# Optimization experiments

Hardware: AMD Instinct MI355X
Metric: run time of the kernel (lower is better)

Reference implementation:

```python
import jax, jax.numpy as jnp
import numpy as np

N = 100000   # nodes
E = 800000   # edges
D_IN = 128   # input feature dim
H = 128      # GCN hidden units
M = 256      # MLP hidden
L = 40       # num_labels


def setup_inputs() -> dict:
    key = jax.random.key(0)
    ks = jax.random.split(key, 16)
    inp = {
        "x": jax.random.normal(ks[0], (N, D_IN), dtype=jnp.float32),
        "edge_index": jax.random.randint(ks[1], (2, E), 0, N, dtype=jnp.int32),
        "edge_weight": jax.random.uniform(ks[2], (E,), dtype=jnp.float32),
    }
    def glorot(k, shape):
        lim = np.sqrt(6.0 / (shape[0] + shape[1])).astype(np.float32)
        return jax.random.uniform(k, shape, jnp.float32, -lim, lim)
    inp["W0"] = glorot(ks[3], (D_IN, H)); inp["b0"] = jnp.zeros((H,), jnp.float32)
    inp["W1"] = glorot(ks[4], (H, H));    inp["b1"] = jnp.zeros((H,), jnp.float32)
    inp["W2"] = glorot(ks[5], (H, H));    inp["b2"] = jnp.zeros((H,), jnp.float32)
    inp["Wm0"] = glorot(ks[6], (H, M));   inp["bm0"] = jnp.zeros((M,), jnp.float32)
    inp["Wm1"] = glorot(ks[7], (M, L));   inp["bm1"] = jnp.zeros((L,), jnp.float32)
    return inp


def _gcn_norm(edge_index, edge_weight):
    # renorm trick: add self-loops (weight 1.0), then sym-normalize
    loop = jnp.arange(N, dtype=edge_index.dtype)
    row = jnp.concatenate([edge_index[0], loop])
    col = jnp.concatenate([edge_index[1], loop])
    w = jnp.concatenate([edge_weight, jnp.ones((N,), edge_weight.dtype)])
    deg = jax.ops.segment_sum(w, row, num_segments=N)
    dinv = jnp.where(deg > 0, jax.lax.rsqrt(deg), 0.0)
    norm = dinv[row] * w * dinv[col]
    return row, col, norm


def _gcn_layer(h, row, col, norm, W, b):
    h = h @ W                                   # [N, H]
    msg = h[col] * norm[:, None]                # gather + scale, [E+N, H]
    agg = jax.ops.segment_sum(msg, row, num_segments=N)
    return jax.nn.relu(agg + b)


def reference(x, edge_index, edge_weight, W0, b0, W1, b1, W2, b2, Wm0, bm0, Wm1, bm1):
    row, col, norm = _gcn_norm(edge_index, edge_weight)
    h = _gcn_layer(x, row, col, norm, W0, b0)
    h = _gcn_layer(h, row, col, norm, W1, b1)
    h = _gcn_layer(h, row, col, norm, W2, b2)
    h = jax.nn.relu(h @ Wm0 + bm0)              # MLP hidden
    return h @ Wm1 + bm1                        # logits [N, L]
```

## Files before the change

### kernel.cpp

```cpp
#include <hip/hip_runtime.h>
#include <hip/hip_fp16.h>
#include <math.h>

#define CAP 32
typedef unsigned short ushort_t;
typedef __attribute__((ext_vector_type(8))) short bf16x8;
typedef __attribute__((ext_vector_type(4))) float f32x4;

__device__ inline float bf2f_lo(unsigned u) { return __uint_as_float(u << 16); }
__device__ inline float bf2f_hi(unsigned u) { return __uint_as_float(u & 0xffff0000u); }
__device__ inline unsigned bf16rne(float f) {
    unsigned u = __float_as_uint(f);
    return (u + 0x7fffu + ((u >> 16) & 1u)) >> 16;
}
__device__ inline float dec_w(unsigned p) {
    return __half2float(__ushort_as_half((ushort_t)(p & 0x7fffu)));
}
__device__ inline bf16x8 u4_to_bf(uint4 u) {
    union { uint4 u; bf16x8 b; } cv; cv.u = u; return cv.b;
}
__device__ inline void accum8(float acc[8], uint4 u, float nm) {
    acc[0] = fmaf(bf2f_lo(u.x), nm, acc[0]);
    acc[1] = fmaf(bf2f_hi(u.x), nm, acc[1]);
    acc[2] = fmaf(bf2f_lo(u.y), nm, acc[2]);
    acc[3] = fmaf(bf2f_hi(u.y), nm, acc[3]);
    acc[4] = fmaf(bf2f_lo(u.z), nm, acc[4]);
    acc[5] = fmaf(bf2f_hi(u.z), nm, acc[5]);
    acc[6] = fmaf(bf2f_lo(u.w), nm, acc[6]);
    acc[7] = fmaf(bf2f_hi(u.w), nm, acc[7]);
}

__global__ __launch_bounds__(256) void k_setup0(const float* __restrict__ W0,
    ushort_t* __restrict__ W0t)
{
    int idx = blockIdx.x * 256 + threadIdx.x;
    if (idx < 128 * 128) {
        int k = idx >> 7, c = idx & 127;
        W0t[c * 128 + k] = (ushort_t)bf16rne(W0[idx]);
    }
}

__global__ __launch_bounds__(256) void k_prep2(const unsigned* __restrict__ bucket,
    const int* __restrict__ cursor, float* __restrict__ dinv, int n)
{
    int gid = blockIdx.x * 256 + threadIdx.x;
    int node = gid >> 4;
    if (node >= n) return;
    int f = gid & 15;
    int c = cursor[node]; if (c > CAP) c = CAP;
    float d = 0.f;
    int j0 = 2 * f;
    uint2 p = *(const uint2*)(bucket + (size_t)node * CAP + j0);
    if (j0 < c)     d += dec_w(p.x);
    if (j0 + 1 < c) d += dec_w(p.y);
    #pragma unroll
    for (int m = 1; m < 16; m <<= 1) d += __shfl_xor(d, m, 16);
    if (f == 0) dinv[node] = 1.0f / sqrtf(1.0f + d);
}

__global__ __launch_bounds__(256, 4) void k_fill_gemm1(
    const int* __restrict__ erow, const int* __restrict__ ecol,
    const float* __restrict__ ew, int* __restrict__ cursor,
    unsigned* __restrict__ bucket, int e,
    const float* __restrict__ x, const ushort_t* __restrict__ Wt,
    ushort_t* __restrict__ Cb, int n, int nbg, int K,
    const float* __restrict__ W1, const float* __restrict__ W2,
    const float* __restrict__ Wm0, const float* __restrict__ Wm1,
    ushort_t* __restrict__ W1t, ushort_t* __restrict__ W2t,
    ushort_t* __restrict__ Wm0t, ushort_t* __restrict__ Wm1t,
    int nbe_blk, int ntb)
{
    __shared__ ushort_t Wsb[128 * 128];
    const int tid = threadIdx.x;
    const int bid = blockIdx.x;
    if (bid % K != 0) {
        int fb = bid - bid / K - 1;
        if (fb < nbe_blk) {
            int i = fb * 256 + tid;
            if (i < e) {
                int r = erow[i];
                int pos = atomicAdd(&cursor[r], 1);
                if (pos < CAP) {
                    unsigned hb = (unsigned)__half_as_ushort(__float2half(ew[i]));
                    bucket[(size_t)r * CAP + pos] = ((unsigned)ecol[i] << 15) | hb;
                }
            }
        } else {
            const int S0 = 128 * 128, S1 = 128 * 256, S2 = 256 * 40;
            int total2 = 2 * S0 + S1 + S2;
            int tb = fb - nbe_blk;
            for (int idx = tb * 256 + tid; idx < total2; idx += ntb * 256) {
                int i = idx;
                const float* W; ushort_t* Wt2; int KK, NN;
                if (i < S0)            { W = W1;  Wt2 = W1t;  KK = 128; NN = 128; }
                else if (i < 2 * S0)   { W = W2;  Wt2 = W2t;  KK = 128; NN = 128; i -= S0; }
                else if (i < 2 * S0 + S1) { W = Wm0; Wt2 = Wm0t; KK = 128; NN = 256; i -= 2 * S0; }
                else                   { W = Wm1; Wt2 = Wm1t; KK = 256; NN = 40;  i -= 2 * S0 + S1; }
                int k = i / NN, c = i - k * NN;
                Wt2[(size_t)c * KK + k] = (ushort_t)bf16rne(W[(size_t)k * NN + c]);
            }
        }
        return;
    }
    const int gb = bid / K;
    if (gb >= nbg) return;
    const int row0 = gb * 128;
    {
        const int rl = tid >> 4, ch = tid & 15;
        #pragma unroll
        for (int it = 0; it < 8; ++it) {
            int c = it * 16 + rl;
            uint4 u = *(const uint4*)(Wt + (size_t)c * 128 + ch * 8);
            *(uint4*)&Wsb[(c * 128 + ch * 8) ^ ((c & 7) << 3)] = u;
        }
    }
    __syncthreads();

    const int lane = tid & 63;
    const int wv = tid >> 6;
    const int lm = lane & 15;
    const int lk = (lane >> 4) * 8;
    int g0 = row0 + wv * 32 + lm;
    int g1 = g0 + 16;
    size_t x0 = (size_t)((g0 < n) ? g0 : 0) * 128;
    size_t x1 = (size_t)((g1 < n) ? g1 : 0) * 128;

    f32x4 acc[2][8];
    #pragma unroll
    for (int m = 0; m < 2; ++m)
        #pragma unroll
        for (int t = 0; t < 8; ++t) acc[m][t] = (f32x4){0.f, 0.f, 0.f, 0.f};

    #pragma unroll
    for (int kk = 0; kk < 4; ++kk) {
        int k0 = kk * 32 + lk;
        const float4* s0 = (const float4*)(x + x0 + k0);
        const float4* s1 = (const float4*)(x + x1 + k0);
        float4 v0 = s0[0], v1 = s0[1], v2 = s1[0], v3 = s1[1];
        uint4 p0, p1;
        p0.x = bf16rne(v0.x) | (bf16rne(v0.y) << 16);
        p0.y = bf16rne(v0.z) | (bf16rne(v0.w) << 16);
        p0.z = bf16rne(v1.x) | (bf16rne(v1.y) << 16);
        p0.w = bf16rne(v1.z) | (bf16rne(v1.w) << 16);
        p1.x = bf16rne(v2.x) | (bf16rne(v2.y) << 16);
        p1.y = bf16rne(v2.z) | (bf16rne(v2.w) << 16);
        p1.z = bf16rne(v3.x) | (bf16rne(v3.y) << 16);
        p1.w = bf16rne(v3.z) | (bf16rne(v3.w) << 16);
        bf16x8 a0 = u4_to_bf(p0), a1 = u4_to_bf(p1);
        #pragma unroll
        for (int t = 0; t < 8; ++t) {
            int c = t * 16 + lm;
            bf16x8 b = *(const bf16x8*)&Wsb[(c * 128 + k0) ^ ((c & 7) << 3)];
            acc[0][t] = __builtin_amdgcn_mfma_f32_16x16x32_bf16(a0, b, acc[0][t], 0, 0, 0);
            acc[1][t] = __builtin_amdgcn_mfma_f32_16x16x32_bf16(a1, b, acc[1][t], 0, 0, 0);
        }
    }
    #pragma unroll
    for (int m = 0; m < 2; ++m) {
        #pragma unroll
        for (int j = 0; j < 4; ++j) {
            int gr = row0 + wv * 32 + m * 16 + (lane >> 4) * 4 + j;
            if (gr < n) {
                #pragma unroll
                for (int t = 0; t < 8; ++t)
                    Cb[(size_t)gr * 128 + t * 16 + lm] = (ushort_t)bf16rne(acc[m][t][j]);
            }
        }
    }
}

__global__ __launch_bounds__(256) void k_agg(const ushort_t* __restrict__ hWb,
    const int* __restrict__ cnt, const unsigned* __restrict__ bucket,
    const float* __restrict__ dinv, const float* __restrict__ preb,
    ushort_t* __restrict__ outb, int n)
{
    int gid = blockIdx.x * 256 + threadIdx.x;
    int node = gid >> 4;
    if (node >= n) return;
    int f8 = gid & 15;
    int c = cnt[node]; if (c > CAP) c = CAP;
    size_t s = (size_t)node * CAP, t = s + c;
    float dn = dinv[node];
    float acc[8];
    #pragma unroll
    for (int i = 0; i < 8; ++i) acc[i] = 0.f;
    {
        uint4 v = *(const uint4*)(hWb + (size_t)node * 128 + f8 * 8);
        accum8(acc, v, dn);
    }
    size_t j = s;
    for (; j + 3 < t; j += 4) {
        uint4 q = *(const uint4*)(bucket + j);
        uint4 u0 = *(const uint4*)(hWb + (size_t)(q.x >> 15) * 128 + f8 * 8);
        uint4 u1 = *(const uint4*)(hWb + (size_t)(q.y >> 15) * 128 + f8 * 8);
        uint4 u2 = *(const uint4*)(hWb + (size_t)(q.z >> 15) * 128 + f8 * 8);
        uint4 u3 = *(const uint4*)(hWb + (size_t)(q.w >> 15) * 128 + f8 * 8);
        accum8(acc, u0, dec_w(q.x) * dinv[q.x >> 15]);
        accum8(acc, u1, dec_w(q.y) * dinv[q.y >> 15]);
        accum8(acc, u2, dec_w(q.z) * dinv[q.z >> 15]);
        accum8(acc, u3, dec_w(q.w) * dinv[q.w >> 15]);
    }
    for (; j < t; ++j) {
        unsigned p = bucket[j];
        uint4 u = *(const uint4*)(hWb + (size_t)(p >> 15) * 128 + f8 * 8);
        accum8(acc, u, dec_w(p) * dinv[p >> 15]);
    }
    float4 b0 = *(const float4*)(preb + f8 * 8);
    float4 b1 = *(const float4*)(preb + f8 * 8 + 4);
    uint4 pk;
    pk.x = bf16rne(fmaxf(fmaf(acc[0], dn, b0.x), 0.f))
         | (bf16rne(fmaxf(fmaf(acc[1], dn, b0.y), 0.f)) << 16);
    pk.y = bf16rne(fmaxf(fmaf(acc[2], dn, b0.z), 0.f))
         | (bf16rne(fmaxf(fmaf(acc[3], dn, b0.w), 0.f)) << 16);
    pk.z = bf16rne(fmaxf(fmaf(acc[4], dn, b1.x), 0.f))
         | (bf16rne(fmaxf(fmaf(acc[5], dn, b1.y), 0.f)) << 16);
    pk.w = bf16rne(fmaxf(fmaf(acc[6], dn, b1.z), 0.f))
         | (bf16rne(fmaxf(fmaf(acc[7], dn, b1.w), 0.f)) << 16);
    *(uint4*)(outb + (size_t)node * 128 + f8 * 8) = pk;
}

__global__ __launch_bounds__(256, 4) void k_gemm_bb(
    const ushort_t* __restrict__ Ab, const ushort_t* __restrict__ Wt,
    const float* __restrict__ postb, int postrelu,
    ushort_t* __restrict__ Cb, int cstride, int n)
{
    __shared__ ushort_t Wsb[128 * 128];
    const int row0 = blockIdx.x * 64;
    const int wcol0 = blockIdx.y * 128;
    const float* pbp = postb ? postb + wcol0 : (const float*)0;
    const int tid = threadIdx.x;
    {
        const int rl = tid >> 4, ch = tid & 15;
        #pragma unroll
        for (int it = 0; it < 8; ++it) {
            int c = it * 16 + rl;
            uint4 u = *(const uint4*)(Wt + (size_t)(wcol0 + c) * 128 + ch * 8);
            *(uint4*)&Wsb[(c * 128 + ch * 8) ^ ((c & 7) << 3)] = u;
        }
    }
    __syncthreads();

    const int lane = tid & 63;
    const int wv = tid >> 6;
    const int lm = lane & 15;
    const int lk = (lane >> 4) * 8;
    int g0 = row0 + wv * 16 + lm;
    size_t a0base = (size_t)((g0 < n) ? g0 : 0) * 128;

    f32x4 acc[8];
    #pragma unroll
    for (int t = 0; t < 8; ++t) acc[t] = (f32x4){0.f, 0.f, 0.f, 0.f};

    #pragma unroll
    for (int kk = 0; kk < 4; ++kk) {
        int k0 = kk * 32 + lk;
        bf16x8 a0 = *(const bf16x8*)(Ab + a0base + k0);
        #pragma unroll
        for (int t = 0; t < 8; ++t) {
            int c = t * 16 + lm;
            bf16x8 b = *(const bf16x8*)&Wsb[(c * 128 + k0) ^ ((c & 7) << 3)];
            acc[t] = __builtin_amdgcn_mfma_f32_16x16x32_bf16(a0, b, acc[t], 0, 0, 0);
        }
    }

    float pb[8];
    #pragma unroll
    for (int t = 0; t < 8; ++t) pb[t] = pbp ? pbp[t * 16 + lm] : 0.f;

    #pragma unroll
    for (int j = 0; j < 4; ++j) {
        int gr = row0 + wv * 16 + (lane >> 4) * 4 + j;
        if (gr < n) {
            #pragma unroll
            for (int t = 0; t < 8; ++t) {
                float o = acc[t][j] + pb[t];
                if (postrelu) o = fmaxf(o, 0.f);
                Cb[(size_t)gr * cstride + wcol0 + t * 16 + lm] = (ushort_t)bf16rne(o);
            }
        }
    }
}

__global__ __launch_bounds__(256) void k_final_mfma(
    const ushort_t* __restrict__ hidb, const ushort_t* __restrict__ Wt,
    const float* __restrict__ bias, float* __restrict__ C, int n)
{
    __shared__ ushort_t Asb[64 * 64];
    const int row0 = blockIdx.x * 64;
    const int tid = threadIdx.x;
    const int lane = tid & 63;
    const int wv = tid >> 6;
    const int lm = lane & 15;
    const int lk8 = (lane >> 4) * 8;

    bf16x8 wfrag[3][8];
    #pragma unroll
    for (int t = 0; t < 3; ++t) {
        int col = t * 16 + lm;
        #pragma unroll
        for (int ks = 0; ks < 8; ++ks) {
            if (col < 40)
                wfrag[t][ks] = *(const bf16x8*)(Wt + (size_t)col * 256 + ks * 32 + lk8);
            else
                wfrag[t][ks] = (bf16x8){0, 0, 0, 0, 0, 0, 0, 0};
        }
    }

    f32x4 acc[3];
    #pragma unroll
    for (int t = 0; t < 3; ++t) acc[t] = (f32x4){0.f, 0.f, 0.f, 0.f};

    for (int kb = 0; kb < 256; kb += 64) {
        __syncthreads();
        #pragma unroll
        for (int it = 0; it < 2; ++it) {
            int i = tid + it * 256;
            int r = i >> 3, ch = i & 7;
            int gr = row0 + r;
            uint4 u = make_uint4(0, 0, 0, 0);
            if (gr < n) u = *(const uint4*)(hidb + (size_t)gr * 256 + kb + ch * 8);
            *(uint4*)&Asb[(r * 64 + ch * 8) ^ ((r & 7) << 3)] = u;
        }
        __syncthreads();
        #pragma unroll
        for (int ks = 0; ks < 2; ++ks) {
            int k0 = ks * 32 + lk8;
            int ksg = (kb >> 5) + ks;
            int r = wv * 16 + lm;
            bf16x8 a = *(const bf16x8*)&Asb[(r * 64 + k0) ^ ((r & 7) << 3)];
            #pragma unroll
            for (int t = 0; t < 3; ++t)
                acc[t] = __builtin_amdgcn_mfma_f32_16x16x32_bf16(
                    a, wfrag[t][ksg], acc[t], 0, 0, 0);
        }
    }

    int grb = row0 + wv * 16 + (lane >> 4) * 4;
    #pragma unroll
    for (int t = 0; t < 3; ++t) {
        int col = t * 16 + lm;
        if (col < 40) {
            float pb = bias[col];
            #pragma unroll
            for (int j = 0; j < 4; ++j) {
                int gr = grb + j;
                if (gr < n) C[(size_t)gr * 40 + col] = acc[t][j] + pb;
            }
        }
    }
}


extern "C" void kernel_launch(void* const* d_in, const int* in_sizes, int n_in,
                              void* d_out, int out_size, void* d_ws, size_t ws_size,
                              hipStream_t stream)
{
    const float* x   = (const float*)d_in[0];
    const int*   ei  = (const int*)d_in[1];
    const float* ew  = (const float*)d_in[2];
    const float* W0  = (const float*)d_in[3];
    const float* b0  = (const float*)d_in[4];
    const float* W1  = (const float*)d_in[5];
    const float* b1  = (const float*)d_in[6];
    const float* W2  = (const float*)d_in[7];
    const float* b2  = (const float*)d_in[8];
    const float* Wm0 = (const float*)d_in[9];
    const float* bm0 = (const float*)d_in[10];
    const float* Wm1 = (const float*)d_in[11];
    const float* bm1 = (const float*)d_in[12];
    float* out = (float*)d_out;

    const int n = in_sizes[0] / 128;
    const int e = in_sizes[2];
    const int* erow = ei;
    const int* ecol = ei + e;

    char* ws = (char*)d_ws;
    size_t actB = (size_t)n * 128 * sizeof(ushort_t);
    size_t hidB = (size_t)n * 256 * sizeof(ushort_t);
    size_t bktB = (size_t)n * CAP * 4;
    size_t wtElems = (size_t)3 * 128 * 128 + 256 * 128 + 40 * 256;
    size_t need = 2 * actB + hidB + bktB + (size_t)2 * n * 4 + wtElems * 2;
    if (ws_size < need) return;

    ushort_t* B1     = (ushort_t*)ws;
    ushort_t* B2     = (ushort_t*)(ws + actB);
    ushort_t* hidb   = (ushort_t*)(ws + 2 * actB);
    unsigned* bucket = (unsigned*)(ws + 2 * actB + hidB);
    float*    dinv   = (float*)(ws + 2 * actB + hidB + bktB);
    int*      cursor = (int*)(dinv + n);
    ushort_t* W0t    = (ushort_t*)(cursor + n);
    ushort_t* W1t    = W0t + 128 * 128;
    ushort_t* W2t    = W1t + 128 * 128;
    ushort_t* Wm0t   = W2t + 128 * 128;
    ushort_t* Wm1t   = Wm0t + 256 * 128;

    dim3 blk(256);
    int nb_pn = (n * 16 + 255) / 256;
    int nb_agg = (n * 16 + 255) / 256;
    int nb_g = (n + 127) / 128;
    int nb_g64 = (n + 63) / 64;
    int nbe_blk = (e + 255) / 256;

    hipMemsetAsync(cursor, 0, (size_t)n * 4, stream);
    k_setup0<<<64, blk, 0, stream>>>(W0, W0t);

    int K = nbe_blk / nb_g + 2;
    int TBwant = 128;
    int B = nb_g * K;
    while (B - (B + K - 1) / K < nbe_blk + TBwant) B += K;
    int ntb = (B - (B + K - 1) / K) - nbe_blk;
    k_fill_gemm1<<<B, blk, 0, stream>>>(erow, ecol, ew, cursor, bucket, e,
                                        x, W0t, B1, n, nb_g, K,
                                        W1, W2, Wm0, Wm1, W1t, W2t, Wm0t, Wm1t,
                                        nbe_blk, ntb);
    k_prep2<<<nb_pn, blk, 0, stream>>>(bucket, cursor, dinv, n);

    k_agg<<<nb_agg, blk, 0, stream>>>(B1, cursor, bucket, dinv, b0, B2, n);
    k_gemm_bb<<<dim3(nb_g64, 1), blk, 0, stream>>>(B2, W1t, nullptr, 0, B1, 128, n);
    k_agg<<<nb_agg, blk, 0, stream>>>(B1, cursor, bucket, dinv, b1, B2, n);
    k_gemm_bb<<<dim3(nb_g64, 1), blk, 0, stream>>>(B2, W2t, nullptr, 0, B1, 128, n);
    k_agg<<<nb_agg, blk, 0, stream>>>(B1, cursor, bucket, dinv, b2, B2, n);
    k_gemm_bb<<<dim3(nb_g64, 2), blk, 0, stream>>>(B2, Wm0t, bm0, 1, hidb, 256, n);
    k_final_mfma<<<nb_g64, blk, 0, stream>>>(hidb, Wm1t, bm1, out, n);
}
```

Measured before the change: 262.4 us.

## Quantize GEMM outputs to int8 with per-row scales for gather-heavy aggregation

GEMM outputs that feed neighbour aggregation are now stored as int8 with a per-row absmax scale instead of bf16. The scale is folded with the source node's dinv so the gather loop multiplies by a single scalar per edge. This halves the bytes each random neighbour gather moves in the bandwidth-bound aggregation kernels. To keep the packed-channel layout consistent, the weight transposes permute the K index and the aggregation output and bias are written in that interleaved order. The cost is int8 quantization error in the intermediate activations, which may fall outside the accuracy tolerance.

```diff
diff --git a/kernel.cpp b/kernel.cpp
--- a/kernel.cpp
+++ b/kernel.cpp
@@ -4,11 +4,11 @@
 
 #define CAP 32
 typedef unsigned short ushort_t;
+typedef unsigned char uchar_t;
 typedef __attribute__((ext_vector_type(8))) short bf16x8;
 typedef __attribute__((ext_vector_type(4))) float f32x4;
 
-__device__ inline float bf2f_lo(unsigned u) { return __uint_as_float(u << 16); }
-__device__ inline float bf2f_hi(unsigned u) { return __uint_as_float(u & 0xffff0000u); }
+
 __device__ inline unsigned bf16rne(float f) {
     unsigned u = __float_as_uint(f);
     return (u + 0x7fffu + ((u >> 16) & 1u)) >> 16;
@@ -19,15 +19,31 @@
 __device__ inline bf16x8 u4_to_bf(uint4 u) {
     union { uint4 u; bf16x8 b; } cv; cv.u = u; return cv.b;
 }
-__device__ inline void accum8(float acc[8], uint4 u, float nm) {
-    acc[0] = fmaf(bf2f_lo(u.x), nm, acc[0]);
-    acc[1] = fmaf(bf2f_hi(u.x), nm, acc[1]);
-    acc[2] = fmaf(bf2f_lo(u.y), nm, acc[2]);
-    acc[3] = fmaf(bf2f_hi(u.y), nm, acc[3]);
-    acc[4] = fmaf(bf2f_lo(u.z), nm, acc[4]);
-    acc[5] = fmaf(bf2f_hi(u.z), nm, acc[5]);
-    acc[6] = fmaf(bf2f_lo(u.w), nm, acc[6]);
-    acc[7] = fmaf(bf2f_hi(u.w), nm, acc[7]);
+__device__ inline void accum8i(float acc[8], uint2 u, float nm) {
+    #pragma unroll
+    for (int i = 0; i < 4; ++i)
+        acc[i] = fmaf((float)(signed char)((u.x >> (8 * i)) & 0xffu), nm, acc[i]);
+    #pragma unroll
+    for (int i = 0; i < 4; ++i)
+        acc[4 + i] = fmaf((float)(signed char)((u.y >> (8 * i)) & 0xffu), nm, acc[4 + i]);
+}
+
+__device__ inline void quant_store(const float o[8], float inv, uchar_t* dst)
+{
+    unsigned lo = 0, hi = 0;
+    #pragma unroll
+    for (int t = 0; t < 4; ++t) {
+        int q = __float2int_rn(o[t] * inv);
+        q = (q > 127) ? 127 : ((q < -127) ? -127 : q);
+        lo |= ((unsigned)(q & 0xff)) << (8 * t);
+    }
+    #pragma unroll
+    for (int t = 4; t < 8; ++t) {
+        int q = __float2int_rn(o[t] * inv);
+        q = (q > 127) ? 127 : ((q < -127) ? -127 : q);
+        hi |= ((unsigned)(q & 0xff)) << (8 * (t - 4));
+    }
+    *(uint2*)dst = make_uint2(lo, hi);
 }
 
 __global__ __launch_bounds__(256) void k_setup0(const float* __restrict__ W0,
@@ -41,7 +57,8 @@
 }
 
 __global__ __launch_bounds__(256) void k_prep2(const unsigned* __restrict__ bucket,
-    const int* __restrict__ cursor, float* __restrict__ dinv, int n)
+    const int* __restrict__ cursor, float* __restrict__ dinv,
+    float* __restrict__ srow, int n)
 {
     int gid = blockIdx.x * 256 + threadIdx.x;
     int node = gid >> 4;
@@ -55,7 +72,11 @@
     if (j0 + 1 < c) d += dec_w(p.y);
     #pragma unroll
     for (int m = 1; m < 16; m <<= 1) d += __shfl_xor(d, m, 16);
-    if (f == 0) dinv[node] = 1.0f / sqrtf(1.0f + d);
+    if (f == 0) {
+        float di = 1.0f / sqrtf(1.0f + d);
+        dinv[node] = di;
+        srow[node] *= di;
+    }
 }
 
 __global__ __launch_bounds__(256, 4) void k_fill_gemm1(
@@ -63,7 +84,7 @@
     const float* __restrict__ ew, int* __restrict__ cursor,
     unsigned* __restrict__ bucket, int e,
     const float* __restrict__ x, const ushort_t* __restrict__ Wt,
-    ushort_t* __restrict__ Cb, int n, int nbg, int K,
+    uchar_t* __restrict__ C8, float* __restrict__ srow, int n, int nbg, int K,
     const float* __restrict__ W1, const float* __restrict__ W2,
     const float* __restrict__ Wm0, const float* __restrict__ Wm1,
     ushort_t* __restrict__ W1t, ushort_t* __restrict__ W2t,
@@ -91,13 +112,14 @@
             int tb = fb - nbe_blk;
             for (int idx = tb * 256 + tid; idx < total2; idx += ntb * 256) {
                 int i = idx;
-                const float* W; ushort_t* Wt2; int KK, NN;
-                if (i < S0)            { W = W1;  Wt2 = W1t;  KK = 128; NN = 128; }
-                else if (i < 2 * S0)   { W = W2;  Wt2 = W2t;  KK = 128; NN = 128; i -= S0; }
-                else if (i < 2 * S0 + S1) { W = Wm0; Wt2 = Wm0t; KK = 128; NN = 256; i -= 2 * S0; }
-                else                   { W = Wm1; Wt2 = Wm1t; KK = 256; NN = 40;  i -= 2 * S0 + S1; }
+                const float* W; ushort_t* Wt2; int KK, NN, perm;
+                if (i < S0)            { W = W1;  Wt2 = W1t;  KK = 128; NN = 128; perm = 1; }
+                else if (i < 2 * S0)   { W = W2;  Wt2 = W2t;  KK = 128; NN = 128; perm = 1; i -= S0; }
+                else if (i < 2 * S0 + S1) { W = Wm0; Wt2 = Wm0t; KK = 128; NN = 256; perm = 1; i -= 2 * S0; }
+                else                   { W = Wm1; Wt2 = Wm1t; KK = 256; NN = 40;  perm = 0; i -= 2 * S0 + S1; }
                 int k = i / NN, c = i - k * NN;
-                Wt2[(size_t)c * KK + k] = (ushort_t)bf16rne(W[(size_t)k * NN + c]);
+                int kp = perm ? (((k & 15) << 3) | (k >> 4)) : k;
+                Wt2[(size_t)c * KK + kp] = (ushort_t)bf16rne(W[(size_t)k * NN + c]);
             }
         }
         return;
@@ -159,20 +181,28 @@
     for (int m = 0; m < 2; ++m) {
         #pragma unroll
         for (int j = 0; j < 4; ++j) {
+            float o[8];
+            #pragma unroll
+            for (int t = 0; t < 8; ++t) o[t] = acc[m][t][j];
+            float mx = 0.f;
+            #pragma unroll
+            for (int t = 0; t < 8; ++t) mx = fmaxf(mx, fabsf(o[t]));
+            #pragma unroll
+            for (int s = 1; s < 16; s <<= 1) mx = fmaxf(mx, __shfl_xor(mx, s, 16));
+            float inv = (mx > 0.f) ? 127.0f / mx : 0.f;
             int gr = row0 + wv * 32 + m * 16 + (lane >> 4) * 4 + j;
             if (gr < n) {
-                #pragma unroll
-                for (int t = 0; t < 8; ++t)
-                    Cb[(size_t)gr * 128 + t * 16 + lm] = (ushort_t)bf16rne(acc[m][t][j]);
-            }
-        }
-    }
-}
-
-__global__ __launch_bounds__(256) void k_agg(const ushort_t* __restrict__ hWb,
+                quant_store(o, inv, C8 + (size_t)gr * 128 + lm * 8);
+                if (lm == 0) srow[gr] = mx * (1.0f / 127.0f);
+            }
+        }
+    }
+}
+
+__global__ __launch_bounds__(256) void k_agg(const uchar_t* __restrict__ hW8,
     const int* __restrict__ cnt, const unsigned* __restrict__ bucket,
-    const float* __restrict__ dinv, const float* __restrict__ preb,
-    ushort_t* __restrict__ outb, int n)
+    const float* __restrict__ dinv, const float* __restrict__ srow,
+    const float* __restrict__ preb, ushort_t* __restrict__ outb, int n)
 {
     int gid = blockIdx.x * 256 + threadIdx.x;
     int node = gid >> 4;
@@ -185,44 +215,46 @@
     #pragma unroll
     for (int i = 0; i < 8; ++i) acc[i] = 0.f;
     {
-        uint4 v = *(const uint4*)(hWb + (size_t)node * 128 + f8 * 8);
-        accum8(acc, v, dn);
+        uint2 v = *(const uint2*)(hW8 + (size_t)node * 128 + f8 * 8);
+        accum8i(acc, v, srow[node]);
     }
     size_t j = s;
     for (; j + 3 < t; j += 4) {
         uint4 q = *(const uint4*)(bucket + j);
-        uint4 u0 = *(const uint4*)(hWb + (size_t)(q.x >> 15) * 128 + f8 * 8);
-        uint4 u1 = *(const uint4*)(hWb + (size_t)(q.y >> 15) * 128 + f8 * 8);
-        uint4 u2 = *(const uint4*)(hWb + (size_t)(q.z >> 15) * 128 + f8 * 8);
-        uint4 u3 = *(const uint4*)(hWb + (size_t)(q.w >> 15) * 128 + f8 * 8);
-        accum8(acc, u0, dec_w(q.x) * dinv[q.x >> 15]);
-        accum8(acc, u1, dec_w(q.y) * dinv[q.y >> 15]);
-        accum8(acc, u2, dec_w(q.z) * dinv[q.z >> 15]);
-        accum8(acc, u3, dec_w(q.w) * dinv[q.w >> 15]);
+        int c0 = q.x >> 15, c1 = q.y >> 15, c2 = q.z >> 15, c3 = q.w >> 15;
+        uint2 u0 = *(const uint2*)(hW8 + (size_t)c0 * 128 + f8 * 8);
+        uint2 u1 = *(const uint2*)(hW8 + (size_t)c1 * 128 + f8 * 8);
+        uint2 u2 = *(const uint2*)(hW8 + (size_t)c2 * 128 + f8 * 8);
+        uint2 u3 = *(const uint2*)(hW8 + (size_t)c3 * 128 + f8 * 8);
+        accum8i(acc, u0, dec_w(q.x) * srow[c0]);
+        accum8i(acc, u1, dec_w(q.y) * srow[c1]);
+        accum8i(acc, u2, dec_w(q.z) * srow[c2]);
+        accum8i(acc, u3, dec_w(q.w) * srow[c3]);
     }
     for (; j < t; ++j) {
         unsigned p = bucket[j];
-        uint4 u = *(const uint4*)(hWb + (size_t)(p >> 15) * 128 + f8 * 8);
-        accum8(acc, u, dec_w(p) * dinv[p >> 15]);
-    }
-    float4 b0 = *(const float4*)(preb + f8 * 8);
-    float4 b1 = *(const float4*)(preb + f8 * 8 + 4);
+        int cc = p >> 15;
+        uint2 u = *(const uint2*)(hW8 + (size_t)cc * 128 + f8 * 8);
+        accum8i(acc, u, dec_w(p) * srow[cc]);
+    }
+    float o[8];
+    #pragma unroll
+    for (int i = 0; i < 8; ++i)
+        o[i] = fmaxf(fmaf(acc[i], dn, preb[(i << 4) | f8]), 0.f);
     uint4 pk;
-    pk.x = bf16rne(fmaxf(fmaf(acc[0], dn, b0.x), 0.f))
-         | (bf16rne(fmaxf(fmaf(acc[1], dn, b0.y), 0.f)) << 16);
-    pk.y = bf16rne(fmaxf(fmaf(acc[2], dn, b0.z), 0.f))
-         | (bf16rne(fmaxf(fmaf(acc[3], dn, b0.w), 0.f)) << 16);
-    pk.z = bf16rne(fmaxf(fmaf(acc[4], dn, b1.x), 0.f))
-         | (bf16rne(fmaxf(fmaf(acc[5], dn, b1.y), 0.f)) << 16);
-    pk.w = bf16rne(fmaxf(fmaf(acc[6], dn, b1.z), 0.f))
-         | (bf16rne(fmaxf(fmaf(acc[7], dn, b1.w), 0.f)) << 16);
+    pk.x = bf16rne(o[0]) | (bf16rne(o[1]) << 16);
+    pk.y = bf16rne(o[2]) | (bf16rne(o[3]) << 16);
+    pk.z = bf16rne(o[4]) | (bf16rne(o[5]) << 16);
+    pk.w = bf16rne(o[6]) | (bf16rne(o[7]) << 16);
     *(uint4*)(outb + (size_t)node * 128 + f8 * 8) = pk;
 }
 
 __global__ __launch_bounds__(256, 4) void k_gemm_bb(
     const ushort_t* __restrict__ Ab, const ushort_t* __restrict__ Wt,
     const float* __restrict__ postb, int postrelu,
-    ushort_t* __restrict__ Cb, int cstride, int n)
+    ushort_t* __restrict__ Cb, int cstride,
+    uchar_t* __restrict__ C8, float* __restrict__ srow,
+    const float* __restrict__ dinv, int n)
 {
     __shared__ ushort_t Wsb[128 * 128];
     const int row0 = blockIdx.x * 64;
@@ -263,19 +295,38 @@
         }
     }
 
-    float pb[8];
-    #pragma unroll
-    for (int t = 0; t < 8; ++t) pb[t] = pbp ? pbp[t * 16 + lm] : 0.f;
-
-    #pragma unroll
-    for (int j = 0; j < 4; ++j) {
-        int gr = row0 + wv * 16 + (lane >> 4) * 4 + j;
-        if (gr < n) {
-            #pragma unroll
-            for (int t = 0; t < 8; ++t) {
-                float o = acc[t][j] + pb[t];
-                if (postrelu) o = fmaxf(o, 0.f);
-                Cb[(size_t)gr * cstride + wcol0 + t * 16 + lm] = (ushort_t)bf16rne(o);
+    if (C8) {
+        #pragma unroll
+        for (int j = 0; j < 4; ++j) {
+            float o[8];
+            #pragma unroll
+            for (int t = 0; t < 8; ++t) o[t] = acc[t][j];
+            float mx = 0.f;
+            #pragma unroll
+            for (int t = 0; t < 8; ++t) mx = fmaxf(mx, fabsf(o[t]));
+            #pragma unroll
+            for (int s = 1; s < 16; s <<= 1) mx = fmaxf(mx, __shfl_xor(mx, s, 16));
+            float inv = (mx > 0.f) ? 127.0f / mx : 0.f;
+            int gr = row0 + wv * 16 + (lane >> 4) * 4 + j;
+            if (gr < n) {
+                quant_store(o, inv, C8 + (size_t)gr * 128 + lm * 8);
+                if (lm == 0) srow[gr] = mx * (1.0f / 127.0f) * dinv[gr];
+            }
+        }
+    } else {
+        float pb[8];
+        #pragma unroll
+        for (int t = 0; t < 8; ++t) pb[t] = pbp ? pbp[t * 16 + lm] : 0.f;
+        #pragma unroll
+        for (int j = 0; j < 4; ++j) {
+            int gr = row0 + wv * 16 + (lane >> 4) * 4 + j;
+            if (gr < n) {
+                #pragma unroll
+                for (int t = 0; t < 8; ++t) {
+                    float o = acc[t][j] + pb[t];
+                    if (postrelu) o = fmaxf(o, 0.f);
+                    Cb[(size_t)gr * cstride + wcol0 + t * 16 + lm] = (ushort_t)bf16rne(o);
+                }
             }
         }
     }
@@ -376,19 +427,22 @@
     const int* ecol = ei + e;
 
     char* ws = (char*)d_ws;
-    size_t actB = (size_t)n * 128 * sizeof(ushort_t);
+    size_t actB_ = (size_t)n * 128 * sizeof(ushort_t);
     size_t hidB = (size_t)n * 256 * sizeof(ushort_t);
+    size_t h8B = (size_t)n * 128;
     size_t bktB = (size_t)n * CAP * 4;
     size_t wtElems = (size_t)3 * 128 * 128 + 256 * 128 + 40 * 256;
-    size_t need = 2 * actB + hidB + bktB + (size_t)2 * n * 4 + wtElems * 2;
+    size_t need = 2 * actB_ + hidB + h8B + bktB + (size_t)3 * n * 4 + wtElems * 2;
     if (ws_size < need) return;
 
-    ushort_t* B1     = (ushort_t*)ws;
-    ushort_t* B2     = (ushort_t*)(ws + actB);
-    ushort_t* hidb   = (ushort_t*)(ws + 2 * actB);
-    unsigned* bucket = (unsigned*)(ws + 2 * actB + hidB);
-    float*    dinv   = (float*)(ws + 2 * actB + hidB + bktB);
-    int*      cursor = (int*)(dinv + n);
+    ushort_t* actA   = (ushort_t*)ws;
+    ushort_t* actBp  = (ushort_t*)(ws + actB_);
+    ushort_t* hidb   = (ushort_t*)(ws + 2 * actB_);
+    uchar_t*  hW8    = (uchar_t*)(ws + 2 * actB_ + hidB);
+    unsigned* bucket = (unsigned*)(ws + 2 * actB_ + hidB + h8B);
+    float*    dinv   = (float*)(ws + 2 * actB_ + hidB + h8B + bktB);
+    float*    srow   = dinv + n;
+    int*      cursor = (int*)(srow + n);
     ushort_t* W0t    = (ushort_t*)(cursor + n);
     ushort_t* W1t    = W0t + 128 * 128;
     ushort_t* W2t    = W1t + 128 * 128;
@@ -411,16 +465,19 @@
     while (B - (B + K - 1) / K < nbe_blk + TBwant) B += K;
     int ntb = (B - (B + K - 1) / K) - nbe_blk;
     k_fill_gemm1<<<B, blk, 0, stream>>>(erow, ecol, ew, cursor, bucket, e,
-                                        x, W0t, B1, n, nb_g, K,
+                                        x, W0t, hW8, srow, n, nb_g, K,
                                         W1, W2, Wm0, Wm1, W1t, W2t, Wm0t, Wm1t,
                                         nbe_blk, ntb);
-    k_prep2<<<nb_pn, blk, 0, stream>>>(bucket, cursor, dinv, n);
-
-    k_agg<<<nb_agg, blk, 0, stream>>>(B1, cursor, bucket, dinv, b0, B2, n);
-    k_gemm_bb<<<dim3(nb_g64, 1), blk, 0, stream>>>(B2, W1t, nullptr, 0, B1, 128, n);
-    k_agg<<<nb_agg, blk, 0, stream>>>(B1, cursor, bucket, dinv, b1, B2, n);
-    k_gemm_bb<<<dim3(nb_g64, 1), blk, 0, stream>>>(B2, W2t, nullptr, 0, B1, 128, n);
-    k_agg<<<nb_agg, blk, 0, stream>>>(B1, cursor, bucket, dinv, b2, B2, n);
-    k_gemm_bb<<<dim3(nb_g64, 2), blk, 0, stream>>>(B2, Wm0t, bm0, 1, hidb, 256, n);
+    k_prep2<<<nb_pn, blk, 0, stream>>>(bucket, cursor, dinv, srow, n);
+
+    k_agg<<<nb_agg, blk, 0, stream>>>(hW8, cursor, bucket, dinv, srow, b0, actA, n);
+    k_gemm_bb<<<dim3(nb_g64, 1), blk, 0, stream>>>(actA, W1t, nullptr, 0,
+                                                   nullptr, 0, hW8, srow, dinv, n);
+    k_agg<<<nb_agg, blk, 0, stream>>>(hW8, cursor, bucket, dinv, srow, b1, actBp, n);
+    k_gemm_bb<<<dim3(nb_g64, 1), blk, 0, stream>>>(actBp, W2t, nullptr, 0,
+                                                   nullptr, 0, hW8, srow, dinv, n);
+    k_agg<<<nb_agg, blk, 0, stream>>>(hW8, cursor, bucket, dinv, srow, b2, actA, n);
+    k_gemm_bb<<<dim3(nb_g64, 2), blk, 0, stream>>>(actA, Wm0t, bm0, 1,
+                                                   hidb, 256, nullptr, nullptr, nullptr, n);
     k_final_mfma<<<nb_g64, blk, 0, stream>>>(hidb, Wm1t, bm1, out, n);
 }
```

Result: faster. 231.0 us, median of 2 (-12.0%).
